# Performance work log

Measured on AMD Instinct MI355X. Metric: run time of the kernel, lower is better.

The kernel has to match this reference:

```python
import jax, jax.numpy as jnp
import numpy as np


def setup_inputs() -> dict:
    key = jax.random.key(0)
    ks = jax.random.split(key, 16)
    B, P, N, E = 16, 12, 20000, 320000
    f32 = jnp.float32
    x = jax.random.normal(ks[0], (B, P, N), f32)
    input_mask = (jax.random.uniform(ks[1], (B, P, N)) > 0.2).astype(f32)  # GAIN observed mask
    noise = jax.random.uniform(ks[2], (B, P, N), f32) * 0.01  # Uniform(0, 0.01) noise matrix
    edge_index = jax.random.randint(ks[3], (2, E), 0, N)
    edge_weights = jax.random.uniform(ks[4], (E,), f32)

    def lin(k, fi, fo):
        return jax.random.normal(k, (fi, fo), f32) * (1.0 / np.sqrt(fi))

    params = dict(
        Wz=lin(ks[5], 2, P), bz=jnp.zeros((P,), f32),
        Wr=lin(ks[6], 2, P), br=jnp.zeros((P,), f32),
        Wh=lin(ks[7], 2, P), bh=jnp.zeros((P,), f32),
        Lz_w=lin(ks[8], 2 * P, P), Lz_b=jnp.zeros((P,), f32),
        Lr_w=lin(ks[9], 2 * P, P), Lr_b=jnp.zeros((P,), f32),
        Lh_w=lin(ks[10], 2 * P, P), Lh_b=jnp.zeros((P,), f32),
        attention=jax.random.uniform(ks[11], (P,), f32),
        W1=lin(ks[12], P, P), b1=jnp.zeros((P,), f32),
        W2=lin(ks[13], P, P), b2=jnp.zeros((P,), f32),
    )
    return dict(x=x, input_mask=input_mask, noise=noise,
                edge_index=edge_index, edge_weights=edge_weights, **params)


def reference(x, input_mask, noise, edge_index, edge_weights,
              Wz, bz, Wr, br, Wh, bh,
              Lz_w, Lz_b, Lr_w, Lr_b, Lh_w, Lh_b,
              attention, W1, b1, W2, b2):
    B, P, N = x.shape
    # GAIN: fill missing entries with small uniform noise
    x = input_mask * x + (1.0 - input_mask) * noise
    # stack([x, mask]) -> [2,B,P,N]; permute(1,3,0,2) -> [B,N,2,P]; we scan over periods
    X = jnp.transpose(jnp.stack([x, input_mask], axis=2), (1, 0, 3, 2))  # [P, B, N, 2]

    # GCNConv symmetric normalization with self-loops (fill_value = 1)
    src, dst = edge_index[0], edge_index[1]
    loop = jnp.arange(N)
    src_sl = jnp.concatenate([src, loop])
    dst_sl = jnp.concatenate([dst, loop])
    w_sl = jnp.concatenate([edge_weights, jnp.ones((N,), x.dtype)])
    deg = jnp.zeros((N,), x.dtype).at[dst_sl].add(w_sl)
    dinv = jnp.where(deg > 0, deg ** -0.5, 0.0)
    norm = dinv[src_sl] * w_sl * dinv[dst_sl]  # [E + N]

    probs = jax.nn.softmax(attention)  # attention over periods
    H0 = jnp.zeros((B, N, P), x.dtype)  # A3TGCN2 never updates H -> each period sees H = 0

    def step(acc, inp):
        Xt, p = inp  # Xt: [B, N, 2]
        # aggregate raw 2-dim features then apply the (linear) GCN weight: same math,
        # far cheaper than gathering the projected [B, E, P] messages
        msgs = Xt[:, src_sl, :] * norm[None, :, None]          # [B, E+N, 2]
        agg = jnp.zeros_like(Xt).at[:, dst_sl, :].add(msgs)    # [B, N, 2]
        xz = agg @ Wz + bz
        xr = agg @ Wr + br
        xh = agg @ Wh + bh
        Z = jax.nn.sigmoid(jnp.concatenate([xz, H0], axis=-1) @ Lz_w + Lz_b)
        R = jax.nn.sigmoid(jnp.concatenate([xr, H0], axis=-1) @ Lr_w + Lr_b)
        Ht = jnp.tanh(jnp.concatenate([xh, H0 * R], axis=-1) @ Lh_w + Lh_b)
        H = Z * H0 + (1.0 - Z) * Ht
        return acc + p * H, None

    H_accum, _ = jax.lax.scan(step, H0, (X, probs))  # [B, N, P]

    # MLP head: ReLU -> Linear -> ReLU -> Linear -> Sigmoid
    h = jax.nn.relu(H_accum)
    h = jax.nn.relu(h @ W1 + b1)
    imput = jax.nn.sigmoid(h @ W2 + b2)               # [B, N, P]
    imputation = jnp.transpose(imput, (0, 2, 1))      # [B, P, N]
    res = input_mask * x + (1.0 - input_mask) * imputation
    return res, imputation
```

## Files before the change

kernel.cpp:

```cpp
#include <hip/hip_runtime.h>

#define NN 20000
#define NE 320000
#define BB 16
#define PP 12
#define NCOL 384
#define OUT_OFF (BB*PP*NN)
#define SLICES 8
#define SCOLS 48

__device__ __forceinline__ float sigmoidf_(float v) {
    return __fdividef(1.f, 1.f + __expf(-v));
}
__device__ __forceinline__ float tanh_fast(float v) {
    v = fminf(fmaxf(v, -15.f), 15.f);
    float e = __expf(-2.f * v);
    return __fdividef(1.f - e, 1.f + e);
}

__global__ __launch_bounds__(256) void init_kernel(float* deg, int* cnt) {
    int i = blockIdx.x * 256 + threadIdx.x;
    if (i < NN) { deg[i] = 1.0f; cnt[i] = 0; }
}

__global__ __launch_bounds__(256) void degcnt_kernel(const int* __restrict__ ei,
                                                     const float* __restrict__ ew,
                                                     float* deg, int* cnt) {
    int e = blockIdx.x * 256 + threadIdx.x;
    if (e < NE) {
        int d = ei[NE + e];
        atomicAdd(&deg[d], ew[e]);
        atomicAdd(&cnt[d], 1);
    }
}

__global__ __launch_bounds__(1024) void scan_kernel(const int* __restrict__ cnt,
                                                    const float* __restrict__ deg,
                                                    int* __restrict__ rowp,
                                                    int* __restrict__ cur,
                                                    float* __restrict__ dinv) {
    __shared__ int lds[1024];
    int tid = threadIdx.x;
    int base = tid * 20;
    int local[20];
    int s = 0;
    #pragma unroll
    for (int k = 0; k < 20; ++k) {
        int i = base + k;
        int v = (i < NN) ? cnt[i] : 0;
        local[k] = s;
        s += v;
    }
    lds[tid] = s;
    __syncthreads();
    for (int off = 1; off < 1024; off <<= 1) {
        int add = (tid >= off) ? lds[tid - off] : 0;
        __syncthreads();
        lds[tid] += add;
        __syncthreads();
    }
    int pre = (tid > 0) ? lds[tid - 1] : 0;
    #pragma unroll
    for (int k = 0; k < 20; ++k) {
        int i = base + k;
        if (i < NN) {
            int ex = pre + local[k];
            rowp[i] = ex; cur[i] = ex;
            float dg = deg[i];
            dinv[i] = dg > 0.f ? 1.0f / sqrtf(dg) : 0.f;
        }
    }
    if (tid == 0) rowp[NN] = lds[1023];
}

__global__ __launch_bounds__(256) void scatter_kernel(const int* __restrict__ ei,
                                                      const float* __restrict__ ew,
                                                      const float* __restrict__ dinv,
                                                      int* cur, int2* __restrict__ epk) {
    int e = blockIdx.x * 256 + threadIdx.x;
    if (e < NE) {
        int s = ei[e];
        int d = ei[NE + e];
        int pos = atomicAdd(&cur[d], 1);
        float v = dinv[s] * ew[e] * dinv[d];
        epk[pos] = make_int2(s, __float_as_int(v));
    }
}

__global__ __launch_bounds__(256) void prep_kernel(const float* __restrict__ Wz, const float* __restrict__ bz,
                                                   const float* __restrict__ Wh, const float* __restrict__ bh,
                                                   const float* __restrict__ Lzw, const float* __restrict__ Lzb,
                                                   const float* __restrict__ Lhw, const float* __restrict__ Lhb,
                                                   const float* __restrict__ att,
                                                   const float* __restrict__ W1, const float* __restrict__ b1,
                                                   const float* __restrict__ W2, const float* __restrict__ b2,
                                                   float* __restrict__ cst) {
    int t = threadIdx.x;
    if (t < PP) {
        int p = t;
        float az0 = 0.f, az1 = 0.f, cz = 0.f, ah0 = 0.f, ah1 = 0.f, ch = 0.f;
        for (int q = 0; q < PP; ++q) {
            float lz = Lzw[q * PP + p], lh = Lhw[q * PP + p];
            az0 += Wz[q] * lz;
            az1 += Wz[PP + q] * lz;
            cz  += bz[q] * lz;
            ah0 += Wh[q] * lh;
            ah1 += Wh[PP + q] * lh;
            ch  += bh[q] * lh;
        }
        cz += Lzb[p]; ch += Lhb[p];
        cst[p] = az0; cst[12 + p] = az1; cst[24 + p] = cz;
        cst[36 + p] = ah0; cst[48 + p] = ah1; cst[60 + p] = ch;
        float m = att[0];
        for (int q = 1; q < PP; ++q) m = fmaxf(m, att[q]);
        float ssum = 0.f;
        for (int q = 0; q < PP; ++q) ssum += __expf(att[q] - m);
        cst[72 + p] = __expf(att[p] - m) / ssum;
    }
    if (t < 144) { cst[84 + t] = W1[t]; cst[240 + t] = W2[t]; }
    if (t < PP) { cst[228 + t] = b1[t]; cst[384 + t] = b2[t]; }
}

#define TILE 32
__global__ __launch_bounds__(256) void buildx_kernel(const float* __restrict__ x,
                                                     const float* __restrict__ mask,
                                                     const float* __restrict__ noise,
                                                     float* __restrict__ X) {
    __shared__ float tile[TILE][NCOL + 1];
    int tid = threadIdx.x;
    int n0 = blockIdx.x * TILE;
    int i = tid & 31;
    int prb = tid >> 5;
    #pragma unroll 4
    for (int it = 0; it < 24; ++it) {
        int pr = it * 8 + prb;
        int g = pr * NN + n0 + i;
        float m = mask[g];
        float xv = x[g];
        float nz = noise[g];
        float xf = m * xv + (1.f - m) * nz;
        int col = pr * 2;
        tile[i][col]     = xf;
        tile[i][col + 1] = m;
    }
    __syncthreads();
    #pragma unroll 4
    for (int it = 0; it < 48; ++it) {
        int idx = it * 256 + tid;
        int r = idx / NCOL;
        int c = idx - r * NCOL;
        X[(n0 + r) * NCOL + c] = tile[r][c];
    }
}

__global__ __launch_bounds__(256) void spmm_kernel(const float* __restrict__ X,
                                                   const float* __restrict__ dinv,
                                                   const int* __restrict__ rowp,
                                                   const long long* __restrict__ ep,
                                                   float* __restrict__ agg) {
    int slice = blockIdx.x & 7;
    int grp   = blockIdx.x >> 3;
    int wave  = threadIdx.x >> 6;
    int lane  = threadIdx.x & 63;
    int d = __builtin_amdgcn_readfirstlane(grp * 4 + wave);
    int c = slice * SCOLS + lane;
    bool act = lane < SCOLS;
    float di = dinv[d];
    float acc = act ? di * di * X[(size_t)d * NCOL + c] : 0.f;
    int r0 = rowp[d];
    int r1 = rowp[d + 1];
    if (r0 < r1) {
        long long q[8], p[8];
        int e = r0;
        #pragma unroll
        for (int k = 0; k < 8; ++k) {
            int ix = e + k; ix = ix < r1 ? ix : r1 - 1;
            q[k] = ep[ix];
        }
        while (e < r1) {
            #pragma unroll
            for (int k = 0; k < 8; ++k) p[k] = q[k];
            int en = e + 8;
            if (en < r1) {
                #pragma unroll
                for (int k = 0; k < 8; ++k) {
                    int ix = en + k; ix = ix < r1 ? ix : r1 - 1;
                    q[k] = ep[ix];
                }
            }
            #pragma unroll
            for (int k = 0; k < 8; ++k) {
                if (e + k < r1) {
                    int s = (int)p[k];
                    float v = __int_as_float((int)(p[k] >> 32));
                    if (act) acc += v * X[(size_t)s * NCOL + c];
                }
            }
            e = en;
        }
    }
    if (act) {
        int b = slice * 2 + (lane >= 24 ? 1 : 0);
        int j = lane - (lane >= 24 ? 24 : 0);
        __builtin_nontemporal_store(acc, &agg[((size_t)b * NN + d) * 24 + j]);
    }
}

__global__ __launch_bounds__(256) void pointwise_kernel(const float* __restrict__ agg,
                                                        const float* __restrict__ cst,
                                                        const float* __restrict__ x,
                                                        const float* __restrict__ mask,
                                                        float* __restrict__ out) {
    __shared__ float C[396];
    int tid = threadIdx.x;
    for (int i = tid; i < 396; i += 256) C[i] = cst[i];
    __syncthreads();
    int idx = blockIdx.x * 256 + tid;
    int b = idx / NN;
    int n = idx - b * NN;
    float A[24];
    const float4* ap = (const float4*)(agg + ((size_t)b * NN + n) * 24);
    #pragma unroll
    for (int k = 0; k < 6; ++k) {
        float4 v = ap[k];
        A[4 * k + 0] = v.x; A[4 * k + 1] = v.y; A[4 * k + 2] = v.z; A[4 * k + 3] = v.w;
    }
    float h1[12];
    #pragma unroll
    for (int p = 0; p < 12; ++p) {
        float az0 = C[p], az1 = C[12 + p], czp = C[24 + p];
        float ah0 = C[36 + p], ah1 = C[48 + p], chp = C[60 + p];
        float hp = 0.f;
        #pragma unroll
        for (int t = 0; t < 12; ++t) {
            float a0 = A[2 * t], a1 = A[2 * t + 1];
            float z  = sigmoidf_(a0 * az0 + a1 * az1 + czp);
            float th = tanh_fast(a0 * ah0 + a1 * ah1 + chp);
            hp += C[72 + t] * ((1.f - z) * th);
        }
        h1[p] = fmaxf(hp, 0.f);
    }
    float h2[12];
    #pragma unroll
    for (int p = 0; p < 12; ++p) {
        float s = C[228 + p];
        #pragma unroll
        for (int q = 0; q < 12; ++q) s += h1[q] * C[84 + q * 12 + p];
        h2[p] = fmaxf(s, 0.f);
    }
    #pragma unroll
    for (int p = 0; p < 12; ++p) {
        float s = C[384 + p];
        #pragma unroll
        for (int q = 0; q < 12; ++q) s += h2[q] * C[240 + q * 12 + p];
        float imp = sigmoidf_(s);
        int o = (b * PP + p) * NN + n;
        float m = mask[o];
        float xv = x[o];
        out[o] = m * xv + (1.f - m) * imp;
        out[OUT_OFF + o] = imp;
    }
}

extern "C" void kernel_launch(void* const* d_in, const int* in_sizes, int n_in,
                              void* d_out, int out_size, void* d_ws, size_t ws_size,
                              hipStream_t stream) {
    const float* x     = (const float*)d_in[0];
    const float* mask  = (const float*)d_in[1];
    const float* noise = (const float*)d_in[2];
    const int*   ei    = (const int*)d_in[3];
    const float* ew    = (const float*)d_in[4];
    const float* Wz    = (const float*)d_in[5];
    const float* bz    = (const float*)d_in[6];
    const float* Wh    = (const float*)d_in[9];
    const float* bh    = (const float*)d_in[10];
    const float* Lzw   = (const float*)d_in[11];
    const float* Lzb   = (const float*)d_in[12];
    const float* Lhw   = (const float*)d_in[15];
    const float* Lhb   = (const float*)d_in[16];
    const float* att   = (const float*)d_in[17];
    const float* W1    = (const float*)d_in[18];
    const float* b1    = (const float*)d_in[19];
    const float* W2    = (const float*)d_in[20];
    const float* b2    = (const float*)d_in[21];
    float* out = (float*)d_out;

    float* Xf   = (float*)d_ws;
    float* AGG  = Xf + (size_t)NN * NCOL;
    long long* EPK = (long long*)(AGG + (size_t)NN * NCOL);
    float* DEG  = (float*)(EPK + NE);
    float* DINV = DEG + NN;
    float* CST  = DINV + NN;
    int*   CNT  = (int*)(CST + 512);
    int*   ROWP = CNT + NN;
    int*   CUR  = ROWP + NN + 1;

    hipLaunchKernelGGL(init_kernel,    dim3((NN + 255) / 256), dim3(256), 0, stream, DEG, CNT);
    hipLaunchKernelGGL(degcnt_kernel,  dim3((NE + 255) / 256), dim3(256), 0, stream, ei, ew, DEG, CNT);
    hipLaunchKernelGGL(scan_kernel,    dim3(1), dim3(1024), 0, stream, CNT, DEG, ROWP, CUR, DINV);
    hipLaunchKernelGGL(scatter_kernel, dim3((NE + 255) / 256), dim3(256), 0, stream, ei, ew, DINV, CUR, (int2*)EPK);
    hipLaunchKernelGGL(prep_kernel,    dim3(1), dim3(256), 0, stream,
                       Wz, bz, Wh, bh, Lzw, Lzb, Lhw, Lhb, att, W1, b1, W2, b2, CST);
    hipLaunchKernelGGL(buildx_kernel,  dim3(NN / TILE), dim3(256), 0, stream, x, mask, noise, Xf);
    hipLaunchKernelGGL(spmm_kernel,    dim3(SLICES * NN / 4), dim3(256), 0, stream, Xf, DINV, ROWP, EPK, AGG);
    hipLaunchKernelGGL(pointwise_kernel, dim3((BB * NN) / 256), dim3(256), 0, stream, AGG, CST, x, mask, out);
}
```

Before: 439.5 us.

## Process four rows per wave in SpMM with shuffled edge records; split buildx tiles

The SpMM kernel now has each wave handle four destination rows. Edge records are loaded cooperatively by 32 lanes and broadcast with shuffles, and the loop runs to the max degree of the four rows so more independent gathers are in flight. Padding entries have zero weight and point at row 0, which costs wasted work when degrees are uneven. The buildx transpose is split across four y-blocks with a smaller LDS tile to raise occupancy. The init and prep kernels are replaced by a memset and a two-block fused scan/prep kernel, with the self-loop weight folded into the rsqrt.

```diff
diff --git a/kernel.cpp b/kernel.cpp
--- a/kernel.cpp
+++ b/kernel.cpp
@@ -18,11 +18,6 @@
     return __fdividef(1.f - e, 1.f + e);
 }
 
-__global__ __launch_bounds__(256) void init_kernel(float* deg, int* cnt) {
-    int i = blockIdx.x * 256 + threadIdx.x;
-    if (i < NN) { deg[i] = 1.0f; cnt[i] = 0; }
-}
-
 __global__ __launch_bounds__(256) void degcnt_kernel(const int* __restrict__ ei,
                                                      const float* __restrict__ ew,
                                                      float* deg, int* cnt) {
@@ -34,13 +29,47 @@
     }
 }
 
-__global__ __launch_bounds__(1024) void scan_kernel(const int* __restrict__ cnt,
-                                                    const float* __restrict__ deg,
-                                                    int* __restrict__ rowp,
-                                                    int* __restrict__ cur,
-                                                    float* __restrict__ dinv) {
+__global__ __launch_bounds__(1024) void scanprep_kernel(const int* __restrict__ cnt,
+                                                        const float* __restrict__ deg,
+                                                        int* __restrict__ rowp,
+                                                        int* __restrict__ cur,
+                                                        float* __restrict__ dinv,
+                                                        const float* __restrict__ Wz, const float* __restrict__ bz,
+                                                        const float* __restrict__ Wh, const float* __restrict__ bh,
+                                                        const float* __restrict__ Lzw, const float* __restrict__ Lzb,
+                                                        const float* __restrict__ Lhw, const float* __restrict__ Lhb,
+                                                        const float* __restrict__ att,
+                                                        const float* __restrict__ W1, const float* __restrict__ b1,
+                                                        const float* __restrict__ W2, const float* __restrict__ b2,
+                                                        float* __restrict__ cst) {
+    int tid = threadIdx.x;
+    if (blockIdx.x == 1) {
+        if (tid < PP) {
+            int p = tid;
+            float az0 = 0.f, az1 = 0.f, cz = 0.f, ah0 = 0.f, ah1 = 0.f, ch = 0.f;
+            for (int q = 0; q < PP; ++q) {
+                float lz = Lzw[q * PP + p], lh = Lhw[q * PP + p];
+                az0 += Wz[q] * lz;
+                az1 += Wz[PP + q] * lz;
+                cz  += bz[q] * lz;
+                ah0 += Wh[q] * lh;
+                ah1 += Wh[PP + q] * lh;
+                ch  += bh[q] * lh;
+            }
+            cz += Lzb[p]; ch += Lhb[p];
+            cst[p] = az0; cst[12 + p] = az1; cst[24 + p] = cz;
+            cst[36 + p] = ah0; cst[48 + p] = ah1; cst[60 + p] = ch;
+            float m = att[0];
+            for (int q = 1; q < PP; ++q) m = fmaxf(m, att[q]);
+            float ssum = 0.f;
+            for (int q = 0; q < PP; ++q) ssum += __expf(att[q] - m);
+            cst[72 + p] = __expf(att[p] - m) / ssum;
+        }
+        if (tid < 144) { cst[84 + tid] = W1[tid]; cst[240 + tid] = W2[tid]; }
+        if (tid < PP)  { cst[228 + tid] = b1[tid]; cst[384 + tid] = b2[tid]; }
+        return;
+    }
     __shared__ int lds[1024];
-    int tid = threadIdx.x;
     int base = tid * 20;
     int local[20];
     int s = 0;
@@ -66,8 +95,7 @@
         if (i < NN) {
             int ex = pre + local[k];
             rowp[i] = ex; cur[i] = ex;
-            float dg = deg[i];
-            dinv[i] = dg > 0.f ? 1.0f / sqrtf(dg) : 0.f;
+            dinv[i] = __frsqrt_rn(deg[i] + 1.0f);
         }
     }
     if (tid == 0) rowp[NN] = lds[1023];
@@ -87,69 +115,37 @@
     }
 }
 
-__global__ __launch_bounds__(256) void prep_kernel(const float* __restrict__ Wz, const float* __restrict__ bz,
-                                                   const float* __restrict__ Wh, const float* __restrict__ bh,
-                                                   const float* __restrict__ Lzw, const float* __restrict__ Lzb,
-                                                   const float* __restrict__ Lhw, const float* __restrict__ Lhb,
-                                                   const float* __restrict__ att,
-                                                   const float* __restrict__ W1, const float* __restrict__ b1,
-                                                   const float* __restrict__ W2, const float* __restrict__ b2,
-                                                   float* __restrict__ cst) {
-    int t = threadIdx.x;
-    if (t < PP) {
-        int p = t;
-        float az0 = 0.f, az1 = 0.f, cz = 0.f, ah0 = 0.f, ah1 = 0.f, ch = 0.f;
-        for (int q = 0; q < PP; ++q) {
-            float lz = Lzw[q * PP + p], lh = Lhw[q * PP + p];
-            az0 += Wz[q] * lz;
-            az1 += Wz[PP + q] * lz;
-            cz  += bz[q] * lz;
-            ah0 += Wh[q] * lh;
-            ah1 += Wh[PP + q] * lh;
-            ch  += bh[q] * lh;
-        }
-        cz += Lzb[p]; ch += Lhb[p];
-        cst[p] = az0; cst[12 + p] = az1; cst[24 + p] = cz;
-        cst[36 + p] = ah0; cst[48 + p] = ah1; cst[60 + p] = ch;
-        float m = att[0];
-        for (int q = 1; q < PP; ++q) m = fmaxf(m, att[q]);
-        float ssum = 0.f;
-        for (int q = 0; q < PP; ++q) ssum += __expf(att[q] - m);
-        cst[72 + p] = __expf(att[p] - m) / ssum;
-    }
-    if (t < 144) { cst[84 + t] = W1[t]; cst[240 + t] = W2[t]; }
-    if (t < PP) { cst[228 + t] = b1[t]; cst[384 + t] = b2[t]; }
-}
-
 #define TILE 32
 __global__ __launch_bounds__(256) void buildx_kernel(const float* __restrict__ x,
                                                      const float* __restrict__ mask,
                                                      const float* __restrict__ noise,
                                                      float* __restrict__ X) {
-    __shared__ float tile[TILE][NCOL + 1];
+    __shared__ float tile[TILE][97];
     int tid = threadIdx.x;
     int n0 = blockIdx.x * TILE;
+    int pr0 = blockIdx.y * 48;
     int i = tid & 31;
     int prb = tid >> 5;
-    #pragma unroll 4
-    for (int it = 0; it < 24; ++it) {
-        int pr = it * 8 + prb;
+    #pragma unroll
+    for (int it = 0; it < 6; ++it) {
+        int prl = it * 8 + prb;
+        int pr = pr0 + prl;
         int g = pr * NN + n0 + i;
         float m = mask[g];
         float xv = x[g];
         float nz = noise[g];
         float xf = m * xv + (1.f - m) * nz;
-        int col = pr * 2;
-        tile[i][col]     = xf;
-        tile[i][col + 1] = m;
+        tile[i][prl * 2]     = xf;
+        tile[i][prl * 2 + 1] = m;
     }
     __syncthreads();
-    #pragma unroll 4
-    for (int it = 0; it < 48; ++it) {
+    int c0 = blockIdx.y * 96;
+    #pragma unroll
+    for (int it = 0; it < 12; ++it) {
         int idx = it * 256 + tid;
-        int r = idx / NCOL;
-        int c = idx - r * NCOL;
-        X[(n0 + r) * NCOL + c] = tile[r][c];
+        int r = idx / 96;
+        int c = idx - r * 96;
+        X[(n0 + r) * NCOL + c0 + c] = tile[r][c];
     }
 }
 
@@ -162,47 +158,66 @@
     int grp   = blockIdx.x >> 3;
     int wave  = threadIdx.x >> 6;
     int lane  = threadIdx.x & 63;
-    int d = __builtin_amdgcn_readfirstlane(grp * 4 + wave);
-    int c = slice * SCOLS + lane;
+    int d0 = (grp * 4 + wave) * 4;
+    int c  = slice * SCOLS + lane;
     bool act = lane < SCOLS;
-    float di = dinv[d];
-    float acc = act ? di * di * X[(size_t)d * NCOL + c] : 0.f;
-    int r0 = rowp[d];
-    int r1 = rowp[d + 1];
-    if (r0 < r1) {
-        long long q[8], p[8];
-        int e = r0;
-        #pragma unroll
-        for (int k = 0; k < 8; ++k) {
-            int ix = e + k; ix = ix < r1 ? ix : r1 - 1;
-            q[k] = ep[ix];
-        }
-        while (e < r1) {
+    int cg = act ? c : slice * SCOLS;
+
+    int r0[4], r1[4];
+    float acc[4];
+    #pragma unroll
+    for (int r = 0; r < 4; ++r) {
+        int d = d0 + r;
+        r0[r] = rowp[d];
+        r1[r] = rowp[d + 1];
+        float di = dinv[d];
+        acc[r] = act ? di * di * X[(size_t)d * NCOL + c] : 0.f;
+    }
+    int maxdeg = max(max(r1[0] - r0[0], r1[1] - r0[1]), max(r1[2] - r0[2], r1[3] - r0[3]));
+
+    int fr0 = 0, fr1 = 0;
+    if (lane < 32) {
+        int fd = d0 + (lane >> 3);
+        fr0 = rowp[fd];
+        fr1 = rowp[fd + 1];
+    }
+    int fj = lane & 7;
+
+    long long cur = 0;
+    {
+        int e = fr0 + fj;
+        if (lane < 32 && e < fr1) cur = __builtin_nontemporal_load(ep + e);
+    }
+    for (int off = 0; off < maxdeg; off += 8) {
+        long long nxt = 0;
+        {
+            int e = fr0 + off + 8 + fj;
+            if (lane < 32 && e < fr1) nxt = __builtin_nontemporal_load(ep + e);
+        }
+        float vv[4][8], xv[4][8];
+        #pragma unroll
+        for (int r = 0; r < 4; ++r) {
             #pragma unroll
-            for (int k = 0; k < 8; ++k) p[k] = q[k];
-            int en = e + 8;
-            if (en < r1) {
-                #pragma unroll
-                for (int k = 0; k < 8; ++k) {
-                    int ix = en + k; ix = ix < r1 ? ix : r1 - 1;
-                    q[k] = ep[ix];
-                }
+            for (int j = 0; j < 8; ++j) {
+                long long rec = __shfl(cur, r * 8 + j);
+                int s = (int)rec;
+                vv[r][j] = __int_as_float((int)(rec >> 32));
+                xv[r][j] = X[(size_t)s * NCOL + cg];
             }
+        }
+        #pragma unroll
+        for (int r = 0; r < 4; ++r)
             #pragma unroll
-            for (int k = 0; k < 8; ++k) {
-                if (e + k < r1) {
-                    int s = (int)p[k];
-                    float v = __int_as_float((int)(p[k] >> 32));
-                    if (act) acc += v * X[(size_t)s * NCOL + c];
-                }
-            }
-            e = en;
-        }
+            for (int j = 0; j < 8; ++j)
+                acc[r] += vv[r][j] * xv[r][j];
+        cur = nxt;
     }
     if (act) {
         int b = slice * 2 + (lane >= 24 ? 1 : 0);
         int j = lane - (lane >= 24 ? 24 : 0);
-        __builtin_nontemporal_store(acc, &agg[((size_t)b * NN + d) * 24 + j]);
+        #pragma unroll
+        for (int r = 0; r < 4; ++r)
+            __builtin_nontemporal_store(acc[r], &agg[((size_t)b * NN + d0 + r) * 24 + j]);
     }
 }
 
@@ -289,19 +304,18 @@
     float* AGG  = Xf + (size_t)NN * NCOL;
     long long* EPK = (long long*)(AGG + (size_t)NN * NCOL);
     float* DEG  = (float*)(EPK + NE);
-    float* DINV = DEG + NN;
+    int*   CNT  = (int*)(DEG + NN);
+    float* DINV = (float*)(CNT + NN);
     float* CST  = DINV + NN;
-    int*   CNT  = (int*)(CST + 512);
-    int*   ROWP = CNT + NN;
+    int*   ROWP = (int*)(CST + 512);
     int*   CUR  = ROWP + NN + 1;
 
-    hipLaunchKernelGGL(init_kernel,    dim3((NN + 255) / 256), dim3(256), 0, stream, DEG, CNT);
+    hipMemsetAsync(DEG, 0, (size_t)2 * NN * 4, stream);
     hipLaunchKernelGGL(degcnt_kernel,  dim3((NE + 255) / 256), dim3(256), 0, stream, ei, ew, DEG, CNT);
-    hipLaunchKernelGGL(scan_kernel,    dim3(1), dim3(1024), 0, stream, CNT, DEG, ROWP, CUR, DINV);
+    hipLaunchKernelGGL(scanprep_kernel, dim3(2), dim3(1024), 0, stream, CNT, DEG, ROWP, CUR, DINV,
+                       Wz, bz, Wh, bh, Lzw, Lzb, Lhw, Lhb, att, W1, b1, W2, b2, CST);
     hipLaunchKernelGGL(scatter_kernel, dim3((NE + 255) / 256), dim3(256), 0, stream, ei, ew, DINV, CUR, (int2*)EPK);
-    hipLaunchKernelGGL(prep_kernel,    dim3(1), dim3(256), 0, stream,
-                       Wz, bz, Wh, bh, Lzw, Lzb, Lhw, Lhb, att, W1, b1, W2, b2, CST);
-    hipLaunchKernelGGL(buildx_kernel,  dim3(NN / TILE), dim3(256), 0, stream, x, mask, noise, Xf);
-    hipLaunchKernelGGL(spmm_kernel,    dim3(SLICES * NN / 4), dim3(256), 0, stream, Xf, DINV, ROWP, EPK, AGG);
+    hipLaunchKernelGGL(buildx_kernel,  dim3(NN / TILE, 4), dim3(256), 0, stream, x, mask, noise, Xf);
+    hipLaunchKernelGGL(spmm_kernel,    dim3(SLICES * NN / 16), dim3(256), 0, stream, Xf, DINV, ROWP, EPK, AGG);
     hipLaunchKernelGGL(pointwise_kernel, dim3((BB * NN) / 256), dim3(256), 0, stream, AGG, CST, x, mask, out);
 }
```

After: 379.8 us. 13.6% less time.
